# Kernel tuning notes

Measured on AMD Instinct MI355X. Metric: run time of the kernel, lower is better.

## Reference

```python
import jax, jax.numpy as jnp
import numpy as np
import itertools

B, T, C, H = 2, 512, 768, 12
HS = C // H                      # head size 64
M = 8                            # dpp_top_m
MIN_SIZE, MAX_SIZE = 2, 3        # subset sizes including token i
TEMP = 1.0                       # dpp_temperature
ALPHA = 1.0                      # dpp_penalty_alpha
SIGN = 1.0                       # minimize_det=False -> +log_det
NEG = -1e30

# Static combination tables over the M top-k candidate slots, lexicographic order.
# Filtering combos that touch i's slot (or padding slots) reproduces
# itertools.combinations(topidx_list) order exactly.
COMBS = [np.array(list(itertools.combinations(range(M), s)), dtype=np.int32)
         for s in range(MIN_SIZE - 1, MAX_SIZE)]  # extra sizes 1 and 2


def _token(i, q_i, k, v):
    Tn = k.shape[0]
    sim = k @ q_i                                   # [T]
    sim = jnp.where(jnp.arange(Tn) <= i, sim, -jnp.inf)  # causal
    _, top_idx = jax.lax.top_k(sim, M)              # [M]
    n_cand = jnp.minimum(M, i + 1)
    slot_valid = jnp.arange(M) < n_cand             # padding slots invalid
    slot_is_i = (top_idx == i) & slot_valid
    scores, outs, valids = [], [], []
    for comb in COMBS:
        slots = jnp.asarray(comb)                   # [nc, s]
        nc, s = comb.shape
        valid = slot_valid[slots].all(axis=1) & (~slot_is_i[slots].any(axis=1))
        idx = jnp.concatenate(
            [jnp.full((nc, 1), i, dtype=top_idx.dtype), top_idx[slots]], axis=1)  # [nc, s+1]
        K = k[idx]                                  # [nc, s+1, hs]
        V = v[idx]
        gram = jnp.einsum('cnd,cmd->cnm', K, K)     # [nc, s+1, s+1]
        det = jnp.linalg.det(gram)
        log_det = jnp.log(jnp.where(valid, det, 1.0) + 1e-6)
        score = SIGN * log_det / float(s + 1) ** ALPHA
        dot = jnp.einsum('cnd,d->cn', K, q_i) / HS ** 0.5
        w = jax.nn.softmax(dot, axis=1)
        out_s = jnp.einsum('cn,cnd->cd', w, V)      # [nc, hs]
        scores.append(jnp.where(valid, score, NEG))
        outs.append(out_s)
        valids.append(valid)
    scores = jnp.concatenate(scores)                # [36]
    outs = jnp.concatenate(outs, axis=0)            # [36, hs]
    has_valid = jnp.concatenate(valids).any()
    probs = jax.nn.softmax(scores / TEMP)
    best = jnp.argmax(probs)
    y_st = outs[best]
    y_soft = probs @ outs
    # straight-through: forward value = y_soft, gradient flows through y_st
    y = y_st + jax.lax.stop_gradient(y_soft - y_st)
    return jnp.where(has_valid, y, v[i])


def _dpp_head(q, k, v):  # q,k,v: [T, hs]
    return jax.vmap(lambda i, qi: _token(i, qi, k, v))(jnp.arange(q.shape[0]), q)


def _forward(x, W_attn, b_attn, W_proj, b_proj):
    Bx, Tx, Cx = x.shape
    qkv = x @ W_attn.T + b_attn                     # [B, T, 3C]
    q, k, v = jnp.split(qkv, 3, axis=2)

    def heads(t):  # [B, T, C] -> [B*H, T, hs]
        return t.reshape(Bx, Tx, H, HS).transpose(0, 2, 1, 3).reshape(Bx * H, Tx, HS)

    y = jax.vmap(_dpp_head)(heads(q), heads(k), heads(v))  # [B*H, T, hs]
    y = y.reshape(Bx, H, Tx, HS).transpose(0, 2, 1, 3).reshape(Bx, Tx, Cx)
    return y @ W_proj.T + b_proj


def setup_inputs() -> dict:
    key = jax.random.key(0)
    k1, k2, k3, k4, k5 = jax.random.split(key, 5)
    return {
        'x': jax.random.normal(k1, (B, T, C), dtype=jnp.float32),
        'W_attn': jax.random.normal(k2, (3 * C, C), dtype=jnp.float32) * 0.02,
        'b_attn': jax.random.normal(k3, (3 * C,), dtype=jnp.float32) * 0.02,
        'W_proj': jax.random.normal(k4, (C, C), dtype=jnp.float32) * 0.02,
        'b_proj': jax.random.normal(k5, (C,), dtype=jnp.float32) * 0.02,
    }


def reference(x, W_attn, b_attn, W_proj, b_proj):
    return _forward(x, W_attn, b_attn, W_proj, b_proj)
```

## Files before the change

kernel.cpp:

```cpp
#include <hip/hip_runtime.h>
#include <math.h>

#define Bn 2
#define Hn 12
#define Tn 512
#define Cn 768
#define HS 64
#define BH 24
#define MTOP 8
#define NCOMB 36
#define NEGV -1e30f

#define NX (Bn * Tn * Cn)
#define NW (3 * Cn * Cn)
#define NP (Cn * Cn)

typedef __bf16 bf16x8 __attribute__((ext_vector_type(8)));
typedef float f32x4 __attribute__((ext_vector_type(4)));

__device__ __constant__ int C_SL0[NCOMB] = {
  0,1,2,3,4,5,6,7,
  0,0,0,0,0,0,0,
  1,1,1,1,1,1,
  2,2,2,2,2,
  3,3,3,3,
  4,4,4,
  5,5,
  6};
__device__ __constant__ int C_SL1[NCOMB] = {
  -1,-1,-1,-1,-1,-1,-1,-1,
  1,2,3,4,5,6,7,
  2,3,4,5,6,7,
  3,4,5,6,7,
  4,5,6,7,
  5,6,7,
  6,7,
  7};

__device__ __constant__ int PA[45] = {
  0,0,0,0,0,0,0,0,0,
  1,1,1,1,1,1,1,1,
  2,2,2,2,2,2,2,
  3,3,3,3,3,3,
  4,4,4,4,4,
  5,5,5,5,
  6,6,6,
  7,7,
  8};
__device__ __constant__ int PB[45] = {
  0,1,2,3,4,5,6,7,8,
  1,2,3,4,5,6,7,8,
  2,3,4,5,6,7,8,
  3,4,5,6,7,8,
  4,5,6,7,8,
  5,6,7,8,
  6,7,8,
  7,8,
  8};

__device__ __constant__ int TI[36] = {
  0,1,1,2,2,2,3,3,3,3,4,4,4,4,4,5,5,5,5,5,5,6,6,6,6,6,6,6,7,7,7,7,7,7,7,7};
__device__ __constant__ int TJ[36] = {
  0,0,1,0,1,2,0,1,2,3,0,1,2,3,4,0,1,2,3,4,5,0,1,2,3,4,5,6,0,1,2,3,4,5,6,7};

__device__ __forceinline__ unsigned short bf_rne(float x) {
    unsigned u = __float_as_uint(x);
    return (unsigned short)((u + 0x7fff + ((u >> 16) & 1)) >> 16);
}
__device__ __forceinline__ float bf_f(unsigned short s) {
    return __uint_as_float(((unsigned)s) << 16);
}

template<int CTRL, int RM>
__device__ __forceinline__ float dpp_add_step(float x) {
    int t = __builtin_amdgcn_update_dpp(0, __float_as_int(x), CTRL, RM, 0xf, false);
    return x + __int_as_float(t);
}
template<int CTRL, int RM>
__device__ __forceinline__ float dpp_max_step(float x) {
    int t = __builtin_amdgcn_update_dpp((int)0xFF800000, __float_as_int(x), CTRL, RM, 0xf, false);
    return fmaxf(x, __int_as_float(t));
}
__device__ __forceinline__ float wave_sum(float x) {
    x = dpp_add_step<0x111, 0xf>(x);
    x = dpp_add_step<0x112, 0xf>(x);
    x = dpp_add_step<0x114, 0xf>(x);
    x = dpp_add_step<0x118, 0xf>(x);
    x = dpp_add_step<0x142, 0xa>(x);
    x = dpp_add_step<0x143, 0xc>(x);
    return __int_as_float(__builtin_amdgcn_readlane(__float_as_int(x), 63));
}
__device__ __forceinline__ float wave_max(float x) {
    x = dpp_max_step<0x111, 0xf>(x);
    x = dpp_max_step<0x112, 0xf>(x);
    x = dpp_max_step<0x114, 0xf>(x);
    x = dpp_max_step<0x118, 0xf>(x);
    x = dpp_max_step<0x142, 0xa>(x);
    x = dpp_max_step<0x143, 0xc>(x);
    return __int_as_float(__builtin_amdgcn_readlane(__float_as_int(x), 63));
}

__global__ __launch_bounds__(256) void conv_all(const float* __restrict__ x,
                                                const float* __restrict__ Wa,
                                                const float* __restrict__ Wp,
                                                unsigned short* __restrict__ xcat,
                                                unsigned short* __restrict__ Wcat,
                                                unsigned short* __restrict__ Wpbf) {
    const int idx = (blockIdx.x * 256 + threadIdx.x) * 2;
    if (idx < NX) {
        int r = idx / Cn, c = idx - r * Cn;
        float2 v = *(const float2*)(x + idx);
        unsigned short h0 = bf_rne(v.x), l0 = bf_rne(v.x - bf_f(h0));
        unsigned short h1 = bf_rne(v.y), l1 = bf_rne(v.y - bf_f(h1));
        unsigned ph = (unsigned)h0 | ((unsigned)h1 << 16);
        unsigned pl = (unsigned)l0 | ((unsigned)l1 << 16);
        size_t base = (size_t)r * 2304 + c;
        *(unsigned*)(xcat + base)        = ph;
        *(unsigned*)(xcat + base + 768)  = ph;
        *(unsigned*)(xcat + base + 1536) = pl;
    } else if (idx < NX + NW) {
        int j = idx - NX;
        int r = j / Cn, c = j - r * Cn;
        float2 v = *(const float2*)(Wa + j);
        unsigned short h0 = bf_rne(v.x), l0 = bf_rne(v.x - bf_f(h0));
        unsigned short h1 = bf_rne(v.y), l1 = bf_rne(v.y - bf_f(h1));
        unsigned ph = (unsigned)h0 | ((unsigned)h1 << 16);
        unsigned pl = (unsigned)l0 | ((unsigned)l1 << 16);
        size_t base = (size_t)r * 2304 + c;
        *(unsigned*)(Wcat + base)        = ph;
        *(unsigned*)(Wcat + base + 1536) = ph;
        *(unsigned*)(Wcat + base + 768)  = pl;
    } else if (idx < NX + NW + NP) {
        int j = idx - NX - NW;
        float2 v = *(const float2*)(Wp + j);
        unsigned short h0 = bf_rne(v.x), h1 = bf_rne(v.y);
        *(unsigned*)(Wpbf + j) = (unsigned)h0 | ((unsigned)h1 << 16);
    }
}

__device__ __forceinline__ void gld16(const unsigned short* g, unsigned short* l) {
    __builtin_amdgcn_global_load_lds(
        (const __attribute__((address_space(1))) unsigned short*)g,
        (__attribute__((address_space(3))) unsigned short*)l, 16, 0, 0);
}

__device__ __forceinline__ void gemm_core(const unsigned short* __restrict__ Ag,
                                          const unsigned short* __restrict__ Bg,
                                          int Kst, int NS,
                                          unsigned short* LB,
                                          f32x4 acc[2][2]) {
    const int tid = threadIdx.x;
    const int wv = tid >> 6, lane = tid & 63;
    const int r0 = tid >> 3;
    const int sg = tid & 7;
    const int gsg = sg ^ (r0 & 7);
    const int m0w = (wv >> 1) * 32;
    const int n0w = (wv & 1) * 32;
    const int fr = lane & 15;
    const int tq = lane >> 4;

    const unsigned short* pa0 = Ag + (size_t)r0 * Kst + gsg * 8;
    const unsigned short* pa1 = Ag + (size_t)(r0 + 32) * Kst + gsg * 8;
    const unsigned short* pb0 = Bg + (size_t)r0 * Kst + gsg * 8;
    const unsigned short* pb1 = Bg + (size_t)(r0 + 32) * Kst + gsg * 8;

    unsigned short* lA = LB + wv * 512;
    unsigned short* lB = LB + 4096 + wv * 512;

    auto issue = [&](int s, int b) {
        const int cb = s * 64;
        unsigned short* a  = lA + b * 8192;
        unsigned short* bb = lB + b * 8192;
        gld16(pa0 + cb, a);
        gld16(pa1 + cb, a + 2048);
        gld16(pb0 + cb, bb);
        gld16(pb1 + cb, bb + 2048);
    };

    auto compute = [&](int b) {
        const unsigned short* Ab = LB + b * 8192;
        const unsigned short* Bb = Ab + 4096;
        #pragma unroll
        for (int ks = 0; ks < 2; ++ks) {
            const int t = ks * 4 + tq;
            bf16x8 af[2], bg[2];
            #pragma unroll
            for (int mi = 0; mi < 2; ++mi) {
                const int row = m0w + 16 * mi + fr;
                af[mi] = *(const bf16x8*)(Ab + row * 64 + (t ^ (row & 7)) * 8);
            }
            #pragma unroll
            for (int ni = 0; ni < 2; ++ni) {
                const int row = n0w + 16 * ni + fr;
                bg[ni] = *(const bf16x8*)(Bb + row * 64 + (t ^ (row & 7)) * 8);
            }
            #pragma unroll
            for (int mi = 0; mi < 2; ++mi)
                #pragma unroll
                for (int ni = 0; ni < 2; ++ni)
                    acc[mi][ni] = __builtin_amdgcn_mfma_f32_16x16x32_bf16(af[mi], bg[ni], acc[mi][ni], 0, 0, 0);
        }
    };

    issue(0, 0);
    issue(1, 1);
    int b = 0;
    for (int s = 0; s < NS; ++s) {
        if (s + 1 < NS) asm volatile("s_waitcnt vmcnt(4)" ::: "memory");
        else            asm volatile("s_waitcnt vmcnt(0)" ::: "memory");
        __builtin_amdgcn_s_barrier();
        if (s + 2 < NS) {
            int bn = b + 2; if (bn >= 3) bn -= 3;
            issue(s + 2, bn);
        }
        compute(b);
        if (++b == 3) b = 0;
    }
}

__global__ __launch_bounds__(256) void mfma_qkv(const unsigned short* __restrict__ xcat,
                                                const unsigned short* __restrict__ Wcat,
                                                const float* __restrict__ bias,
                                                unsigned short* __restrict__ qcat,
                                                unsigned short* __restrict__ kcat,
                                                float* __restrict__ vh) {
    __shared__ __align__(16) unsigned short LB[3 * 8192];
    const int xcd = blockIdx.x & 7;
    const int v = blockIdx.x >> 3;
    int tmi, by;
    if (v < 48) { by = xcd * 3 + (v >> 4); tmi = v & 15; }
    else        { int q = xcd * 24 + (v - 48); by = 24 + (q >> 4); tmi = q & 15; }
    const int tm = tmi * 64;
    const int wv = threadIdx.x >> 6, lane = threadIdx.x & 63;
    const int kq = lane >> 4, r = lane & 15;
    f32x4 acc[2][2] = {};

    if (by < 24) {
        const int tn = by * 64;
        gemm_core(xcat + (size_t)tm * 2304, Wcat + (size_t)tn * 2304, 2304, 36, LB, acc);
        const int part = tn / Cn;
        #pragma unroll
        for (int mi = 0; mi < 2; ++mi) {
            #pragma unroll
            for (int ni = 0; ni < 2; ++ni) {
                #pragma unroll
                for (int rr = 0; rr < 4; ++rr) {
                    int mm = tm + (wv >> 1) * 32 + mi * 16 + kq * 4 + rr;
                    int nn = tn + (wv & 1) * 32 + ni * 16 + r;
                    float val = acc[mi][ni][rr] + bias[nn];
                    int bb = mm >> 9, t = mm & 511;
                    int c = nn - part * Cn;
                    int h = c >> 6, d = c & 63;
                    int bh = bb * Hn + h;
                    unsigned short s1 = bf_rne(val);
                    float r1 = val - bf_f(s1);
                    unsigned short s2 = bf_rne(r1);
                    unsigned short s3 = bf_rne(r1 - bf_f(s2));
                    size_t base = ((size_t)bh * Tn + t) * 384 + d;
                    if (part == 0) {
                        qcat[base]       = s1;
                        qcat[base + 64]  = s1;
                        qcat[base + 192] = s1;
                        qcat[base + 128] = s2;
                        qcat[base + 320] = s2;
                        qcat[base + 256] = s3;
                    } else {
                        kcat[base]       = s1;
                        kcat[base + 128] = s1;
                        kcat[base + 256] = s1;
                        kcat[base + 64]  = s2;
                        kcat[base + 320] = s2;
                        kcat[base + 192] = s3;
                    }
                }
            }
        }
    } else {
        const int hvi = by - 24;
        const int cv = hvi * 64;
        gemm_core(xcat + (size_t)tm * 2304,
                  Wcat + (size_t)(1536 + cv) * 2304, 2304, 12, LB, acc);
        #pragma unroll
        for (int mi = 0; mi < 2; ++mi) {
            #pragma unroll
            for (int ni = 0; ni < 2; ++ni) {
                #pragma unroll
                for (int rr = 0; rr < 4; ++rr) {
                    int mm = tm + (wv >> 1) * 32 + mi * 16 + kq * 4 + rr;
                    int nloc = (wv & 1) * 32 + ni * 16 + r;
                    float val = acc[mi][ni][rr] + bias[1536 + cv + nloc];
                    int bb = mm >> 9, t = mm & 511;
                    int bh = bb * Hn + hvi;
                    vh[((size_t)bh * Tn + t) * HS + nloc] = val;
                }
            }
        }
    }
}

__global__ __launch_bounds__(256) void mfma_sim(const unsigned short* __restrict__ qcat,
                                                const unsigned short* __restrict__ kcat,
                                                float* __restrict__ S) {
    __shared__ __align__(16) unsigned short LB[3 * 8192];
    const int xcd = blockIdx.x & 7;
    const int v = blockIdx.x >> 3;
    const int bh = xcd * 3 + v / 36;
    const int tile = v % 36;
    const int ti = TI[tile], tj = TJ[tile];
    f32x4 acc[2][2] = {};
    gemm_core(qcat + ((size_t)bh * Tn + ti * 64) * 384,
              kcat + ((size_t)bh * Tn + tj * 64) * 384, 384, 6, LB, acc);

    const int wv = threadIdx.x >> 6, lane = threadIdx.x & 63;
    const int kq = lane >> 4, r = lane & 15;
    float* Sp = S + (size_t)bh * 147456 + (size_t)(ti * (ti + 1) / 2 + tj) * 4096;
    #pragma unroll
    for (int mi = 0; mi < 2; ++mi)
        #pragma unroll
        for (int ni = 0; ni < 2; ++ni)
            #pragma unroll
            for (int rr = 0; rr < 4; ++rr) {
                int ml = (wv >> 1) * 32 + mi * 16 + kq * 4 + rr;
                int nl = (wv & 1) * 32 + ni * 16 + r;
                Sp[ml * 64 + nl] = acc[mi][ni][rr];
            }
}

__global__ __launch_bounds__(256) void mfma_proj(const unsigned short* __restrict__ Abf,
                                                 const unsigned short* __restrict__ Bbf,
                                                 const float* __restrict__ bias,
                                                 float* __restrict__ outp) {
    __shared__ __align__(16) unsigned short LB[3 * 8192];
    const int xcd = blockIdx.x & 7;
    const int q = xcd * 24 + (blockIdx.x >> 3);
    const int tm = (q & 15) * 64;
    const int tn = (q >> 4) * 64;
    f32x4 acc[2][2] = {};
    gemm_core(Abf + (size_t)tm * Cn, Bbf + (size_t)tn * Cn, Cn, 12, LB, acc);

    const int wv = threadIdx.x >> 6, lane = threadIdx.x & 63;
    const int kq = lane >> 4, r = lane & 15;
    #pragma unroll
    for (int mi = 0; mi < 2; ++mi)
        #pragma unroll
        for (int ni = 0; ni < 2; ++ni)
            #pragma unroll
            for (int rr = 0; rr < 4; ++rr) {
                int mm = tm + (wv >> 1) * 32 + mi * 16 + kq * 4 + rr;
                int nn = tn + (wv & 1) * 32 + ni * 16 + r;
                outp[(size_t)mm * Cn + nn] = acc[mi][ni][rr] + bias[nn];
            }
}

#define CEF(arr, ia, ib) { \
    float _a = arr[ia], _b = arr[ib]; \
    arr[ia] = fmaxf(_a, _b); arr[ib] = fminf(_a, _b); }

__global__ __launch_bounds__(256, 8) void dpp_kernel(const float* __restrict__ S,
                                                     const unsigned short* __restrict__ kcat,
                                                     const float* __restrict__ vh,
                                                     unsigned short* __restrict__ yb) {
    const int xcd = blockIdx.x & 7;
    const int vb = blockIdx.x >> 3;
    const int bh = xcd * 3 + (vb >> 7);
    const int iblk = vb & 127;
    const int w = threadIdx.x >> 6;
    const int lane = threadIdx.x & 63;
    const int i = iblk * 4 + w;

    __shared__ float KshW[4][9][68];
    __shared__ float VshW[4][9][64];
    __shared__ float Gsh[4][81];
    __shared__ float qdsh[4][9];
    const float* Sbh = S + (size_t)bh * 147456;
    const unsigned short* kc = kcat + (size_t)bh * Tn * 384;
    const float* vbase = vh + (size_t)bh * Tn * HS;

    const int t8 = i >> 6;
    const int tribase = t8 * (t8 + 1) / 2;
    const int rloc = (i & 63) * 64;

    float sv[8];
    #pragma unroll
    for (int rr = 0; rr < 8; ++rr) {
        sv[rr] = -INFINITY;
        if (rr <= t8) {
            int j = rr * 64 + lane;
            float s = Sbh[(size_t)(tribase + rr) * 4096 + rloc + lane];
            sv[rr] = (j <= i) ? s : -INFINITY;
        }
    }
    const float qd0 = Sbh[(size_t)(tribase + t8) * 4096 + rloc + (i & 63)];

    float key[8];
    #pragma unroll
    for (int r = 0; r < 8; ++r) key[r] = sv[r];

    CEF(key,0,1) CEF(key,2,3) CEF(key,4,5) CEF(key,6,7)
    CEF(key,0,2) CEF(key,1,3) CEF(key,4,6) CEF(key,5,7)
    CEF(key,1,2) CEF(key,5,6)
    CEF(key,0,4) CEF(key,1,5) CEF(key,2,6) CEF(key,3,7)
    CEF(key,2,4) CEF(key,3,5)
    CEF(key,1,2) CEF(key,3,4) CEF(key,5,6)

    #pragma unroll
    for (int st = 0; st < 6; ++st) {
        const int off = 1 << st;
        float pk[8];
        #pragma unroll
        for (int r = 0; r < 8; ++r)
            pk[r] = __shfl_xor(key[r], off, 64);
        float t[8];
        #pragma unroll
        for (int r = 0; r < 8; ++r)
            t[r] = fmaxf(key[r], pk[7 - r]);
        CEF(t,0,4) CEF(t,1,5) CEF(t,2,6) CEF(t,3,7)
        CEF(t,0,2) CEF(t,1,3) CEF(t,4,6) CEF(t,5,7)
        CEF(t,0,1) CEF(t,2,3) CEF(t,4,5) CEF(t,6,7)
        #pragma unroll
        for (int r = 0; r < 8; ++r) key[r] = t[r];
    }

    int topi[8];
    {
        unsigned long long used[8] = {0, 0, 0, 0, 0, 0, 0, 0};
        #pragma unroll
        for (int p = 0; p < 8; ++p) {
            float v = key[p];
            int idx = i;
            bool found = false;
            #pragma unroll
            for (int r = 0; r < 8; ++r) {
                unsigned long long m = __ballot(sv[r] == v) & ~used[r];
                if (!found && m != 0ull) {
                    int l = __builtin_ctzll(m);
                    idx = r * 64 + l;
                    used[r] |= (1ull << l);
                    found = true;
                }
            }
            topi[p] = idx;
        }
    }

    #pragma unroll
    for (int a = 0; a < 9; ++a) {
        int t = (a == 0) ? i : topi[a - 1];
        size_t kb = (size_t)t * 384 + lane;
        KshW[w][a][lane] = bf_f(kc[kb]) + bf_f(kc[kb + 64]) + bf_f(kc[kb + 192]);
        VshW[w][a][lane] = vbase[(size_t)t * HS + lane];
    }
    if (lane < 9) {
        float val = qd0;
        #pragma unroll
        for (int p = 0; p < 8; ++p) if (lane == p + 1) val = key[p];
        qdsh[w][lane] = val;
    }

    if (lane < 45) {
        const int a = PA[lane], b = PB[lane];
        const float4* rka = (const float4*)&KshW[w][a][0];
        const float4* rkb = (const float4*)&KshW[w][b][0];
        float acc = 0.f;
        #pragma unroll
        for (int t = 0; t < 16; ++t) {
            float4 fa = rka[t], fb = rkb[t];
            acc += fa.x * fb.x; acc += fa.y * fb.y;
            acc += fa.z * fb.z; acc += fa.w * fb.w;
        }
        Gsh[w][a * 9 + b] = acc;
        Gsh[w][b * 9 + a] = acc;
    }

    const int sl0c = (lane < NCOMB) ? C_SL0[lane] : -1;
    const int sl1c = (lane < NCOMB) ? C_SL1[lane] : -1;
    float score = -INFINITY;
    int ca = 0, cb = 0, sdim = 1;
    {
        const int n_cand = (i + 1 < MTOP) ? (i + 1) : MTOP;
        int vmask = 0;
        #pragma unroll
        for (int s = 0; s < MTOP; ++s)
            if (s < n_cand && topi[s] != i) vmask |= (1 << s);

        if (lane < NCOMB) {
            sdim = (sl1c < 0) ? 1 : 2;
            ca = sl0c + 1;
            cb = (sl1c < 0) ? 0 : sl1c + 1;
            bool valid = ((vmask >> sl0c) & 1);
            if (sdim == 2) valid = valid && ((vmask >> sl1c) & 1);
            float G00 = Gsh[w][0];
            float Gaa = Gsh[w][ca * 9 + ca];
            float G0a = Gsh[w][ca];
            float det;
            if (sdim == 1) {
                det = G00 * Gaa - G0a * G0a;
            } else {
                float G0b = Gsh[w][cb];
                float Gab = Gsh[w][ca * 9 + cb];
                float Gbb = Gsh[w][cb * 9 + cb];
                det = G00 * (Gaa * Gbb - Gab * Gab)
                    - G0a * (G0a * Gbb - Gab * G0b)
                    + G0b * (G0a * Gab - Gaa * G0b);
            }
            score = valid ? (logf(det + 1e-6f) / (float)(sdim + 1)) : NEGV;
        }
    }

    const float mxv = wave_max(score);
    const float ee = (lane < NCOMB) ? expf(score - mxv) : 0.f;
    const float sumv = wave_sum(ee);

    float pwx = 0.f, pwy = 0.f, pwz = 0.f;
    if (lane < NCOMB) {
        float prob = ee / sumv;
        float d0 = qdsh[w][0]  * 0.125f;
        float d1 = qdsh[w][ca] * 0.125f;
        float d2 = (sdim == 2) ? qdsh[w][cb] * 0.125f : -INFINITY;
        float m2 = fmaxf(fmaxf(d0, d1), d2);
        float e0 = expf(d0 - m2), e1 = expf(d1 - m2);
        float e2 = (sdim == 2) ? expf(d2 - m2) : 0.f;
        float inv = prob / (e0 + e1 + e2);
        pwx = e0 * inv; pwy = e1 * inv; pwz = e2 * inv;
    }

    const float c0 = wave_sum(pwx);
    float cs[8];
    #pragma unroll
    for (int s = 0; s < 8; ++s) {
        float contrib = ((sl0c == s) ? pwy : 0.f) + ((sl1c == s) ? pwz : 0.f);
        cs[s] = wave_sum(contrib);
    }

    {
        const bool hasValid = (mxv > -1e29f);
        const float v0 = VshW[w][0][lane];
        float y = v0;
        if (hasValid) {
            y = c0 * v0;
            #pragma unroll
            for (int s = 0; s < 8; ++s)
                y += cs[s] * VshW[w][s + 1][lane];
        }
        const int bb = bh / Hn, h = bh % Hn;
        yb[((size_t)(bb * Tn + i)) * Cn + h * HS + lane] = bf_rne(y);
    }
}

extern "C" void kernel_launch(void* const* d_in, const int* in_sizes, int n_in,
                              void* d_out, int out_size, void* d_ws, size_t ws_size,
                              hipStream_t stream) {
    const float* x      = (const float*)d_in[0];
    const float* W_attn = (const float*)d_in[1];
    const float* b_attn = (const float*)d_in[2];
    const float* W_proj = (const float*)d_in[3];
    const float* b_proj = (const float*)d_in[4];
    float* out = (float*)d_out;

    char* ws = (char*)d_ws;
    float* vh            = (float*)(ws);
    unsigned short* qcat = (unsigned short*)(ws + 3145728);
    unsigned short* kcat = (unsigned short*)(ws + 12582912);
    unsigned short* xcat = (unsigned short*)(ws + 22020096);
    unsigned short* Wcat = (unsigned short*)(ws + 26738688);
    float* S             = (float*)(ws + 26738688);
    unsigned short* ybf  = xcat;
    unsigned short* Wpbf = (unsigned short*)(ws + 40894464);

    conv_all<<<dim3((NX + NW + NP) / 2 / 256), 256, 0, stream>>>(
        x, W_attn, W_proj, xcat, Wcat, Wpbf);

    mfma_qkv<<<dim3(576), 256, 0, stream>>>(xcat, Wcat, b_attn, qcat, kcat, vh);

    mfma_sim<<<dim3(864), 256, 0, stream>>>(qcat, kcat, S);

    dpp_kernel<<<dim3(3072), 256, 0, stream>>>(S, kcat, vh, ybf);

    mfma_proj<<<dim3(192), 256, 0, stream>>>(ybf, Wpbf, b_proj, out);
}
```

Measured before the change: 128.8 us.

## Widen QKV GEMM tile to 64x128, vectorize conversion, fast-path top-k index lookup

The QKV projection GEMM now uses a 64x128 output tile per block (4 MFMA column fragments per wave), which halves the block count and raises A-tile reuse per loaded B tile, at the cost of more LDS and registers per block. The input/weight bf16 split conversion processes four floats per thread with 64-bit stores. In the DPP kernel, when the top-8 keys have no duplicates, index recovery skips the used-mask bookkeeping and does a simpler ballot scan.

```diff
diff --git a/kernel.cpp b/kernel.cpp
--- a/kernel.cpp
+++ b/kernel.cpp
@@ -17,6 +17,7 @@
 
 typedef __bf16 bf16x8 __attribute__((ext_vector_type(8)));
 typedef float f32x4 __attribute__((ext_vector_type(4)));
+typedef unsigned long long u64;
 
 __device__ __constant__ int C_SL0[NCOMB] = {
   0,1,2,3,4,5,6,7,
@@ -106,35 +107,40 @@
                                                 unsigned short* __restrict__ xcat,
                                                 unsigned short* __restrict__ Wcat,
                                                 unsigned short* __restrict__ Wpbf) {
-    const int idx = (blockIdx.x * 256 + threadIdx.x) * 2;
+    const int idx = (blockIdx.x * 256 + threadIdx.x) * 4;
     if (idx < NX) {
         int r = idx / Cn, c = idx - r * Cn;
-        float2 v = *(const float2*)(x + idx);
+        float4 v = *(const float4*)(x + idx);
         unsigned short h0 = bf_rne(v.x), l0 = bf_rne(v.x - bf_f(h0));
         unsigned short h1 = bf_rne(v.y), l1 = bf_rne(v.y - bf_f(h1));
-        unsigned ph = (unsigned)h0 | ((unsigned)h1 << 16);
-        unsigned pl = (unsigned)l0 | ((unsigned)l1 << 16);
+        unsigned short h2 = bf_rne(v.z), l2 = bf_rne(v.z - bf_f(h2));
+        unsigned short h3 = bf_rne(v.w), l3 = bf_rne(v.w - bf_f(h3));
+        u64 ph = (u64)h0 | ((u64)h1 << 16) | ((u64)h2 << 32) | ((u64)h3 << 48);
+        u64 pl = (u64)l0 | ((u64)l1 << 16) | ((u64)l2 << 32) | ((u64)l3 << 48);
         size_t base = (size_t)r * 2304 + c;
-        *(unsigned*)(xcat + base)        = ph;
-        *(unsigned*)(xcat + base + 768)  = ph;
-        *(unsigned*)(xcat + base + 1536) = pl;
+        *(u64*)(xcat + base)        = ph;
+        *(u64*)(xcat + base + 768)  = ph;
+        *(u64*)(xcat + base + 1536) = pl;
     } else if (idx < NX + NW) {
         int j = idx - NX;
         int r = j / Cn, c = j - r * Cn;
-        float2 v = *(const float2*)(Wa + j);
+        float4 v = *(const float4*)(Wa + j);
         unsigned short h0 = bf_rne(v.x), l0 = bf_rne(v.x - bf_f(h0));
         unsigned short h1 = bf_rne(v.y), l1 = bf_rne(v.y - bf_f(h1));
-        unsigned ph = (unsigned)h0 | ((unsigned)h1 << 16);
-        unsigned pl = (unsigned)l0 | ((unsigned)l1 << 16);
+        unsigned short h2 = bf_rne(v.z), l2 = bf_rne(v.z - bf_f(h2));
+        unsigned short h3 = bf_rne(v.w), l3 = bf_rne(v.w - bf_f(h3));
+        u64 ph = (u64)h0 | ((u64)h1 << 16) | ((u64)h2 << 32) | ((u64)h3 << 48);
+        u64 pl = (u64)l0 | ((u64)l1 << 16) | ((u64)l2 << 32) | ((u64)l3 << 48);
         size_t base = (size_t)r * 2304 + c;
-        *(unsigned*)(Wcat + base)        = ph;
-        *(unsigned*)(Wcat + base + 1536) = ph;
-        *(unsigned*)(Wcat + base + 768)  = pl;
+        *(u64*)(Wcat + base)        = ph;
+        *(u64*)(Wcat + base + 1536) = ph;
+        *(u64*)(Wcat + base + 768)  = pl;
     } else if (idx < NX + NW + NP) {
         int j = idx - NX - NW;
-        float2 v = *(const float2*)(Wp + j);
+        float4 v = *(const float4*)(Wp + j);
         unsigned short h0 = bf_rne(v.x), h1 = bf_rne(v.y);
-        *(unsigned*)(Wpbf + j) = (unsigned)h0 | ((unsigned)h1 << 16);
+        unsigned short h2 = bf_rne(v.z), h3 = bf_rne(v.w);
+        *(u64*)(Wpbf + j) = (u64)h0 | ((u64)h1 << 16) | ((u64)h2 << 32) | ((u64)h3 << 48);
     }
 }
 
@@ -218,35 +224,113 @@
     }
 }
 
+__device__ __forceinline__ void gemm_core_w(const unsigned short* __restrict__ Ag,
+                                            const unsigned short* __restrict__ Bg,
+                                            int Kst, int NS,
+                                            unsigned short* LB,
+                                            f32x4 acc[2][4]) {
+    const int tid = threadIdx.x;
+    const int wv = tid >> 6, lane = tid & 63;
+    const int r0 = tid >> 3;
+    const int sg = tid & 7;
+    const int gsg = sg ^ (r0 & 7);
+    const int m0w = (wv >> 1) * 32;
+    const int n0w = (wv & 1) * 64;
+    const int fr = lane & 15;
+    const int tq = lane >> 4;
+
+    const unsigned short* pa0 = Ag + (size_t)r0 * Kst + gsg * 8;
+    const unsigned short* pa1 = Ag + (size_t)(r0 + 32) * Kst + gsg * 8;
+    const unsigned short* pb0 = Bg + (size_t)r0 * Kst + gsg * 8;
+    const unsigned short* pb1 = Bg + (size_t)(r0 + 32) * Kst + gsg * 8;
+    const unsigned short* pb2 = Bg + (size_t)(r0 + 64) * Kst + gsg * 8;
+    const unsigned short* pb3 = Bg + (size_t)(r0 + 96) * Kst + gsg * 8;
+
+    unsigned short* lA = LB + wv * 512;
+    unsigned short* lB = LB + 4096 + wv * 512;
+
+    auto issue = [&](int s, int b) {
+        const int cb = s * 64;
+        unsigned short* a  = lA + b * 12288;
+        unsigned short* bb = lB + b * 12288;
+        gld16(pa0 + cb, a);
+        gld16(pa1 + cb, a + 2048);
+        gld16(pb0 + cb, bb);
+        gld16(pb1 + cb, bb + 2048);
+        gld16(pb2 + cb, bb + 4096);
+        gld16(pb3 + cb, bb + 6144);
+    };
+
+    auto compute = [&](int b) {
+        const unsigned short* Ab = LB + b * 12288;
+        const unsigned short* Bb = Ab + 4096;
+        #pragma unroll
+        for (int ks = 0; ks < 2; ++ks) {
+            const int t = ks * 4 + tq;
+            bf16x8 af[2], bg[4];
+            #pragma unroll
+            for (int mi = 0; mi < 2; ++mi) {
+                const int row = m0w + 16 * mi + fr;
+                af[mi] = *(const bf16x8*)(Ab + row * 64 + (t ^ (row & 7)) * 8);
+            }
+            #pragma unroll
+            for (int ni = 0; ni < 4; ++ni) {
+                const int row = n0w + 16 * ni + fr;
+                bg[ni] = *(const bf16x8*)(Bb + row * 64 + (t ^ (row & 7)) * 8);
+            }
+            #pragma unroll
+            for (int mi = 0; mi < 2; ++mi)
+                #pragma unroll
+                for (int ni = 0; ni < 4; ++ni)
+                    acc[mi][ni] = __builtin_amdgcn_mfma_f32_16x16x32_bf16(af[mi], bg[ni], acc[mi][ni], 0, 0, 0);
+        }
+    };
+
+    issue(0, 0);
+    issue(1, 1);
+    int b = 0;
+    for (int s = 0; s < NS; ++s) {
+        if (s + 1 < NS) asm volatile("s_waitcnt vmcnt(6)" ::: "memory");
+        else            asm volatile("s_waitcnt vmcnt(0)" ::: "memory");
+        __builtin_amdgcn_s_barrier();
+        if (s + 2 < NS) {
+            int bn = b + 2; if (bn >= 3) bn -= 3;
+            issue(s + 2, bn);
+        }
+        compute(b);
+        if (++b == 3) b = 0;
+    }
+}
+
 __global__ __launch_bounds__(256) void mfma_qkv(const unsigned short* __restrict__ xcat,
                                                 const unsigned short* __restrict__ Wcat,
                                                 const float* __restrict__ bias,
                                                 unsigned short* __restrict__ qcat,
                                                 unsigned short* __restrict__ kcat,
                                                 float* __restrict__ vh) {
-    __shared__ __align__(16) unsigned short LB[3 * 8192];
+    __shared__ __align__(16) unsigned short LB[3 * 12288];
     const int xcd = blockIdx.x & 7;
     const int v = blockIdx.x >> 3;
-    int tmi, by;
-    if (v < 48) { by = xcd * 3 + (v >> 4); tmi = v & 15; }
-    else        { int q = xcd * 24 + (v - 48); by = 24 + (q >> 4); tmi = q & 15; }
+    int tnt, tmi, isv;
+    if (v < 24) { int q = xcd * 24 + v;        tnt = q >> 4; tmi = q & 15; isv = 0; }
+    else        { int q = xcd * 12 + (v - 24); tnt = q >> 4; tmi = q & 15; isv = 1; }
     const int tm = tmi * 64;
     const int wv = threadIdx.x >> 6, lane = threadIdx.x & 63;
     const int kq = lane >> 4, r = lane & 15;
-    f32x4 acc[2][2] = {};
-
-    if (by < 24) {
-        const int tn = by * 64;
-        gemm_core(xcat + (size_t)tm * 2304, Wcat + (size_t)tn * 2304, 2304, 36, LB, acc);
-        const int part = tn / Cn;
+    f32x4 acc[2][4] = {};
+
+    if (!isv) {
+        const int ncol0 = tnt * 128;
+        gemm_core_w(xcat + (size_t)tm * 2304, Wcat + (size_t)ncol0 * 2304, 2304, 36, LB, acc);
+        const int part = (tnt >= 6) ? 1 : 0;
         #pragma unroll
         for (int mi = 0; mi < 2; ++mi) {
             #pragma unroll
-            for (int ni = 0; ni < 2; ++ni) {
+            for (int ni = 0; ni < 4; ++ni) {
                 #pragma unroll
                 for (int rr = 0; rr < 4; ++rr) {
                     int mm = tm + (wv >> 1) * 32 + mi * 16 + kq * 4 + rr;
-                    int nn = tn + (wv & 1) * 32 + ni * 16 + r;
+                    int nn = ncol0 + (wv & 1) * 64 + ni * 16 + r;
                     float val = acc[mi][ni][rr] + bias[nn];
                     int bb = mm >> 9, t = mm & 511;
                     int c = nn - part * Cn;
@@ -276,22 +360,22 @@
             }
         }
     } else {
-        const int hvi = by - 24;
-        const int cv = hvi * 64;
-        gemm_core(xcat + (size_t)tm * 2304,
-                  Wcat + (size_t)(1536 + cv) * 2304, 2304, 12, LB, acc);
+        const int cv = tnt * 128;
+        gemm_core_w(xcat + (size_t)tm * 2304,
+                    Wcat + (size_t)(1536 + cv) * 2304, 2304, 12, LB, acc);
         #pragma unroll
         for (int mi = 0; mi < 2; ++mi) {
             #pragma unroll
-            for (int ni = 0; ni < 2; ++ni) {
+            for (int ni = 0; ni < 4; ++ni) {
                 #pragma unroll
                 for (int rr = 0; rr < 4; ++rr) {
                     int mm = tm + (wv >> 1) * 32 + mi * 16 + kq * 4 + rr;
-                    int nloc = (wv & 1) * 32 + ni * 16 + r;
-                    float val = acc[mi][ni][rr] + bias[1536 + cv + nloc];
+                    int nloc = (wv & 1) * 64 + ni * 16 + r;
+                    int c = cv + nloc;
+                    float val = acc[mi][ni][rr] + bias[1536 + c];
                     int bb = mm >> 9, t = mm & 511;
-                    int bh = bb * Hn + hvi;
-                    vh[((size_t)bh * Tn + t) * HS + nloc] = val;
+                    int h = c >> 6, d = c & 63;
+                    vh[((size_t)(bb * Hn + h) * Tn + t) * HS + d] = val;
                 }
             }
         }
@@ -422,7 +506,22 @@
     }
 
     int topi[8];
-    {
+    bool dup = false;
+    #pragma unroll
+    for (int p = 0; p < 7; ++p) dup = dup || (key[p] == key[p + 1]);
+    if (!dup) {
+        #pragma unroll
+        for (int p = 0; p < 8; ++p) {
+            float v = key[p];
+            int idx = i;
+            #pragma unroll
+            for (int r = 7; r >= 0; --r) {
+                unsigned long long m = __ballot(sv[r] == v);
+                if (m != 0ull) idx = r * 64 + __builtin_ctzll(m);
+            }
+            topi[p] = idx;
+        }
+    } else {
         unsigned long long used[8] = {0, 0, 0, 0, 0, 0, 0, 0};
         #pragma unroll
         for (int p = 0; p < 8; ++p) {
@@ -567,10 +666,10 @@
     unsigned short* ybf  = xcat;
     unsigned short* Wpbf = (unsigned short*)(ws + 40894464);
 
-    conv_all<<<dim3((NX + NW + NP) / 2 / 256), 256, 0, stream>>>(
+    conv_all<<<dim3((NX + NW + NP) / 4 / 256), 256, 0, stream>>>(
         x, W_attn, W_proj, xcat, Wcat, Wpbf);
 
-    mfma_qkv<<<dim3(576), 256, 0, stream>>>(xcat, Wcat, b_attn, qcat, kcat, vh);
+    mfma_qkv<<<dim3(288), 256, 0, stream>>>(xcat, Wcat, b_attn, qcat, kcat, vh);
 
     mfma_sim<<<dim3(864), 256, 0, stream>>>(qcat, kcat, S);
 
```

Result: slower. 131.4 us (+2.0%).
